# Performance work log

Hardware: AMD Instinct MI355X
Metric: run time of the kernel (lower is better)

## Reference

```python
import jax, jax.numpy as jnp
import numpy as np

N_E = 1024
E_DIM = 256
TAU = 0.5
BETA = 0.25
LAMB = 0.1
EPS = 1e-10


def setup_inputs() -> dict:
    key = jax.random.key(0)
    k1, k2, k3 = jax.random.split(key, 3)
    z = jax.random.normal(k1, (16, 1024, E_DIM), dtype=jnp.float32)
    # kaiming-normal-initialized codebook (std = sqrt(2 / fan_in))
    emb = jax.random.normal(k2, (N_E, E_DIM), dtype=jnp.float32) * np.sqrt(2.0 / E_DIM)
    u = jax.random.uniform(k3, (16 * 1024, N_E), dtype=jnp.float32)
    return {"z": z, "emb": emb, "u": u}


def reference(z, emb, u):
    zf = z.reshape(-1, E_DIM)                                  # [N, e_dim]
    # squared euclidean distances to each code: ||z||^2 + ||e||^2 - 2 z.e
    d = (jnp.sum(zf * zf, axis=1, keepdims=True)
         + jnp.sum(emb * emb, axis=1)
         - 2.0 * jnp.matmul(zf, emb.T))                        # [N, n_e]
    # gumbel-softmax (hard, straight-through) on logits = -d
    g = -jnp.log(-jnp.log(u + EPS) + EPS)
    y_soft = jax.nn.softmax((-d + g) / TAU, axis=-1)
    idx = jnp.argmax(y_soft, axis=-1)
    y_hard = jax.nn.one_hot(idx, N_E, dtype=y_soft.dtype)
    probs = y_hard + y_soft - jax.lax.stop_gradient(y_soft)    # [N, n_e]
    z_q = jnp.matmul(probs, emb).reshape(z.shape)
    # orthogonality loss on the codebook gram matrix
    gram = jnp.matmul(emb, emb.T)
    ortho = jnp.mean((gram - jnp.eye(N_E, dtype=emb.dtype)) ** 2) / (N_E ** 2)
    emb_loss = jnp.mean((jax.lax.stop_gradient(z_q) - z) ** 2)
    commit = BETA * jnp.mean((z_q - jax.lax.stop_gradient(z)) ** 2)
    loss = emb_loss + BETA * commit + LAMB * ortho
    z_q_st = z + jax.lax.stop_gradient(z_q - z)
    e_mean = jnp.mean(probs, axis=0)
    perplexity = jnp.exp(-jnp.sum(e_mean * jnp.log(e_mean + EPS)))
    return loss, z_q_st, perplexity
```

## Files before the change

kernel.cpp:

```cpp
#include <hip/hip_runtime.h>
#include <math.h>
#include <stdint.h>


#define NROWS 16384
#define NE    1024
#define ED    256
#define EPSF  1e-10f
#define INV2048 4.8828125e-4f
#define BM 64
#define BN 64
#define SCW 68

typedef _Float16 half_t;
typedef __attribute__((ext_vector_type(4))) _Float16 half4;
typedef __attribute__((ext_vector_type(8))) _Float16 half8;
typedef __attribute__((ext_vector_type(16))) float floatx16;
typedef unsigned long long u64;

__device__ __forceinline__ void gl_lds16(const void* g, void* l) {
    __builtin_amdgcn_global_load_lds(
        (const __attribute__((address_space(1))) uint32_t*)g,
        (__attribute__((address_space(3))) uint32_t*)l, 16, 0, 0);
}

__device__ __forceinline__ u64 packMax(float v, int code) {
    unsigned int b   = __float_as_uint(v);
    unsigned int key = (b & 0x80000000u) ? ~b : (b | 0x80000000u);
    return ((u64)key << 32) | (unsigned int)(NE - 1 - code);
}

__global__ __launch_bounds__(256) void vq_prep(
        const float* __restrict__ z, const float* __restrict__ emb,
        half_t* __restrict__ zh, half_t* __restrict__ zl,
        half_t* __restrict__ eh, half_t* __restrict__ el,
        float* __restrict__ enorm, float* __restrict__ znorm,
        u64* __restrict__ best)
{
    const int gid = blockIdx.x * 256 + threadIdx.x;
    const int ZQ4 = NROWS * ED / 4;
    if (gid < ZQ4) {
        const float4 v = ((const float4*)z)[gid];
        const float x[4] = {v.x, v.y, v.z, v.w};
        half4 h, l;
#pragma unroll
        for (int i = 0; i < 4; ++i) {
            const half_t hi = (half_t)x[i];
            h[i] = hi; l[i] = (half_t)((x[i] - (float)hi) * 2048.0f);
        }
        *(half4*)&zh[(size_t)gid * 4] = h;
        *(half4*)&zl[(size_t)gid * 4] = l;
        float s = v.x*v.x + v.y*v.y + v.z*v.z + v.w*v.w;
#pragma unroll
        for (int o = 32; o; o >>= 1) s += __shfl_down(s, o);
        if ((threadIdx.x & 63) == 0) znorm[gid >> 6] = s;
    } else {
        const int eg = gid - ZQ4;
        const float4 v = ((const float4*)emb)[eg];
        const float x[4] = {v.x, v.y, v.z, v.w};
        half4 h, l;
#pragma unroll
        for (int i = 0; i < 4; ++i) {
            const half_t hi = (half_t)x[i];
            h[i] = hi; l[i] = (half_t)((x[i] - (float)hi) * 2048.0f);
        }
        *(half4*)&eh[(size_t)eg * 4] = h;
        *(half4*)&el[(size_t)eg * 4] = l;
        float s = v.x*v.x + v.y*v.y + v.z*v.z + v.w*v.w;
#pragma unroll
        for (int o = 32; o; o >>= 1) s += __shfl_down(s, o);
        if ((threadIdx.x & 63) == 0) enorm[eg >> 6] = s;
        if (eg < NROWS) best[eg] = 0ull;
    }
}

__global__ __launch_bounds__(256, 4) void vq_gemm(
        const half_t* __restrict__ zh, const half_t* __restrict__ zl,
        const half_t* __restrict__ eh, const half_t* __restrict__ el,
        const float* __restrict__ u, const float* __restrict__ enorm,
        u64* __restrict__ best)
{
    __shared__ __align__(16) char smem[32768];
    half_t* Ah = (half_t*)smem;
    half_t* Al = (half_t*)(smem + 8192);
    half_t* Bh = (half_t*)(smem + 16384);
    half_t* Bl = (half_t*)(smem + 24576);
    float (*Sc)[SCW] = (float(*)[SCW])smem;
    u64* parr = (u64*)(smem + 17408);

    const int t    = threadIdx.x;
    const int w    = t >> 6;
    const int lane = t & 63;
    const int lrow = lane & 31;
    const int hw   = lane >> 5;

    const int bid = blockIdx.x;
    const int xcd = bid & 7, c = bid >> 3;
    const int m0 = (xcd * 32 + (c >> 4)) * BM;
    const int n0 = (c & 15) * BN;
    const int wm = (w >> 1) * 32, wn = (w & 1) * 32;

    size_t gaoff[2], gboff[2];
#pragma unroll
    for (int it = 0; it < 2; ++it) {
        const int s = it * 256 + t;
        const int row = s >> 3;
        const int cc = (s & 7) ^ (row & 7);
        gaoff[it] = (size_t)(m0 + row) * ED + cc * 8;
        gboff[it] = (size_t)(n0 + row) * ED + cc * 8;
    }

    auto STAGE = [&](int kc) {
#pragma unroll
        for (int it = 0; it < 2; ++it) {
            const int ldso = (it * 256 + w * 64) * 8;
            gl_lds16(zh + gaoff[it] + kc, Ah + ldso);
            gl_lds16(zl + gaoff[it] + kc, Al + ldso);
            gl_lds16(eh + gboff[it] + kc, Bh + ldso);
            gl_lds16(el + gboff[it] + kc, Bl + ldso);
        }
    };

    floatx16 accH = {};
    floatx16 accX = {};

    STAGE(0);
    for (int kc = 0; kc < ED; kc += 64) {
        __syncthreads();
#pragma unroll
        for (int ks = 0; ks < 4; ++ks) {
            const int cch = ks * 2 + hw;
            const int ar = wm + lrow;
            const int br = wn + lrow;
            const int sa = ar * 8 + (cch ^ (ar & 7));
            const int sb = br * 8 + (cch ^ (br & 7));
            const half8 ah = *(const half8*)&Ah[sa * 8];
            const half8 al = *(const half8*)&Al[sa * 8];
            const half8 bh = *(const half8*)&Bh[sb * 8];
            const half8 bl = *(const half8*)&Bl[sb * 8];
            accH = __builtin_amdgcn_mfma_f32_32x32x16_f16(ah, bh, accH, 0, 0, 0);
            accX = __builtin_amdgcn_mfma_f32_32x32x16_f16(ah, bl, accX, 0, 0, 0);
            accX = __builtin_amdgcn_mfma_f32_32x32x16_f16(al, bh, accX, 0, 0, 0);
        }
        __syncthreads();
        if (kc + 64 < ED) STAGE(kc + 64);
    }

    const int   col0 = n0 + wn + lrow;
    const float en0  = enorm[col0];
#pragma unroll
    for (int r = 0; r < 16; ++r) {
        const int lr = wm + (r & 3) + ((r >> 2) << 3) + (hw << 2);
        const float d  = accH[r] + accX[r] * INV2048;
        const float uv = u[(size_t)(m0 + lr) * NE + col0];
        const float g  = -__logf(-__logf(uv + EPSF) + EPSF);
        Sc[lr][wn + lrow] = 2.f * d - en0 + g;
    }
    __syncthreads();

    {
        const int row = t >> 2;
        const int ch  = (t & 3) << 4;
        float bv = -1e38f; int bc = 0;
#pragma unroll
        for (int q = 0; q < 4; ++q) {
            const float4 v = *(const float4*)&Sc[row][ch + (q << 2)];
            const int cc = n0 + ch + (q << 2);
            if (v.x > bv) { bv = v.x; bc = cc; }
            if (v.y > bv) { bv = v.y; bc = cc + 1; }
            if (v.z > bv) { bv = v.z; bc = cc + 2; }
            if (v.w > bv) { bv = v.w; bc = cc + 3; }
        }
        parr[t] = packMax(bv, bc);
    }
    __syncthreads();
    if (t < 64) {
        const u64 a = parr[(t << 2)],     b = parr[(t << 2) + 1];
        const u64 e = parr[(t << 2) + 2], f = parr[(t << 2) + 3];
        const u64 m1 = a > b ? a : b;
        const u64 m2 = e > f ? e : f;
        atomicMax(&best[m0 + t], m1 > m2 ? m1 : m2);
    }
}

__global__ __launch_bounds__(256) void vq_outstore(
        const float* __restrict__ emb, const u64* __restrict__ best,
        const float* __restrict__ znorm, const float* __restrict__ u,
        float* __restrict__ out)
{
    const int t = threadIdx.x;

    if (blockIdx.x == NROWS / 8) {
        __shared__ int    hist[NE];
        __shared__ double redl[4], redp[4];
        for (int i = t; i < NE; i += 256) hist[i] = 0;
        __syncthreads();

        double lsum = 0.0;
#pragma unroll 8
        for (int r = t; r < NROWS; r += 256) {
            const u64 p = best[r];
            const unsigned int key = (unsigned int)(p >> 32);
            const int code = NE - 1 - (int)(p & 0xFFFFFFFFu);
            atomicAdd(&hist[code], 1);
            const unsigned int b = (key & 0x80000000u) ? (key ^ 0x80000000u) : ~key;
            const float s  = __uint_as_float(b);
            const float uv = u[(size_t)r * NE + code];
            const float g  = -__logf(-__logf(uv + EPSF) + EPSF);
            lsum += (double)(znorm[r] - s + g);
        }
        __syncthreads();

        double psum = 0.0;
        for (int i = t; i < NE; i += 256) {
            const float em = (float)hist[i] / (float)NROWS;
            psum += (double)(em * logf(em + EPSF));
        }
#pragma unroll
        for (int o = 32; o; o >>= 1) { lsum += __shfl_down(lsum, o); psum += __shfl_down(psum, o); }
        if ((t & 63) == 0) { redl[t >> 6] = lsum; redp[t >> 6] = psum; }
        __syncthreads();
        if (t == 0) {
            const double mse = (redl[0] + redl[1] + redl[2] + redl[3])
                               / (double)((size_t)NROWS * ED);
            const double tot = redp[0] + redp[1] + redp[2] + redp[3];
            out[0] = (float)(mse * 1.0625);
            out[1 + (size_t)NROWS * ED] = (float)exp(-tot);
        }
        return;
    }

    __shared__ int ridx[8];
    const int m0 = blockIdx.x * 8;
    if (t < 8)
        ridx[t] = NE - 1 - (int)(best[m0 + t] & 0xFFFFFFFFu);
    __syncthreads();

#pragma unroll
    for (int rr = 0; rr < 8; ++rr) {
        const int j = ridx[rr];
        out[1 + (size_t)(m0 + rr) * ED + t] = emb[(size_t)j * ED + t];
    }
}

extern "C" void kernel_launch(void* const* d_in, const int* in_sizes, int n_in,
                              void* d_out, int out_size, void* d_ws, size_t ws_size,
                              hipStream_t stream) {
    const float* z   = (const float*)d_in[0];
    const float* emb = (const float*)d_in[1];
    const float* u   = (const float*)d_in[2];
    float* out = (float*)d_out;

    float*  enorm    = (float*)((char*)d_ws + 5120);
    u64*    best     = (u64*)((char*)d_ws + 9216);
    float*  znorm    = (float*)((char*)d_ws + 140288);
    const size_t small_end = 205824;

    const size_t zsplit = (size_t)NROWS * ED * 2;
    const size_t esplit = (size_t)NE * ED * 2;
    const bool bigws = ws_size >= small_end + 2 * zsplit + 2 * esplit;

    half_t *zh, *zl, *eh, *el;
    if (bigws) {
        char* big = (char*)d_ws + small_end;
        zh = (half_t*)big;
        zl = (half_t*)(big + zsplit);
        eh = (half_t*)(big + 2 * zsplit);
        el = (half_t*)(big + 2 * zsplit + esplit);
    } else {
        zh = (half_t*)((char*)d_out + 8);
        zl = (half_t*)((char*)d_out + 8 + zsplit);
        eh = (half_t*)((char*)d_ws + small_end);
        el = (half_t*)((char*)d_ws + small_end + esplit);
    }

    vq_prep<<<(NROWS * ED / 4 + NE * ED / 4) / 256, 256, 0, stream>>>(
        z, emb, zh, zl, eh, el, enorm, znorm, best);
    vq_gemm<<<(NROWS / BM) * (NE / BN), 256, 0, stream>>>(
        zh, zl, eh, el, u, enorm, best);
    vq_outstore<<<NROWS / 8 + 1, 256, 0, stream>>>(emb, best, znorm, u, out);
}
```

Before: 185.6 us.

## Distribute loss and histogram work across outstore blocks and add finalize kernel

```diff
diff --git a/kernel.cpp b/kernel.cpp
--- a/kernel.cpp
+++ b/kernel.cpp
@@ -38,38 +38,42 @@
         u64* __restrict__ best)
 {
     const int gid = blockIdx.x * 256 + threadIdx.x;
-    const int ZQ4 = NROWS * ED / 4;
-    if (gid < ZQ4) {
-        const float4 v = ((const float4*)z)[gid];
-        const float x[4] = {v.x, v.y, v.z, v.w};
-        half4 h, l;
-#pragma unroll
-        for (int i = 0; i < 4; ++i) {
+    const int ZQ8 = NROWS * ED / 8;
+    if (gid < ZQ8) {
+        const float4 v0 = ((const float4*)z)[(size_t)gid * 2];
+        const float4 v1 = ((const float4*)z)[(size_t)gid * 2 + 1];
+        const float x[8] = {v0.x, v0.y, v0.z, v0.w, v1.x, v1.y, v1.z, v1.w};
+        half8 h, l;
+        float s = 0.f;
+#pragma unroll
+        for (int i = 0; i < 8; ++i) {
             const half_t hi = (half_t)x[i];
             h[i] = hi; l[i] = (half_t)((x[i] - (float)hi) * 2048.0f);
-        }
-        *(half4*)&zh[(size_t)gid * 4] = h;
-        *(half4*)&zl[(size_t)gid * 4] = l;
-        float s = v.x*v.x + v.y*v.y + v.z*v.z + v.w*v.w;
-#pragma unroll
-        for (int o = 32; o; o >>= 1) s += __shfl_down(s, o);
-        if ((threadIdx.x & 63) == 0) znorm[gid >> 6] = s;
+            s = fmaf(x[i], x[i], s);
+        }
+        *(half8*)&zh[(size_t)gid * 8] = h;
+        *(half8*)&zl[(size_t)gid * 8] = l;
+#pragma unroll
+        for (int o = 16; o; o >>= 1) s += __shfl_down(s, o, 32);
+        if ((threadIdx.x & 31) == 0) znorm[gid >> 5] = s;
     } else {
-        const int eg = gid - ZQ4;
-        const float4 v = ((const float4*)emb)[eg];
-        const float x[4] = {v.x, v.y, v.z, v.w};
-        half4 h, l;
-#pragma unroll
-        for (int i = 0; i < 4; ++i) {
+        const int eg = gid - ZQ8;
+        const float4 v0 = ((const float4*)emb)[(size_t)eg * 2];
+        const float4 v1 = ((const float4*)emb)[(size_t)eg * 2 + 1];
+        const float x[8] = {v0.x, v0.y, v0.z, v0.w, v1.x, v1.y, v1.z, v1.w};
+        half8 h, l;
+        float s = 0.f;
+#pragma unroll
+        for (int i = 0; i < 8; ++i) {
             const half_t hi = (half_t)x[i];
             h[i] = hi; l[i] = (half_t)((x[i] - (float)hi) * 2048.0f);
-        }
-        *(half4*)&eh[(size_t)eg * 4] = h;
-        *(half4*)&el[(size_t)eg * 4] = l;
-        float s = v.x*v.x + v.y*v.y + v.z*v.z + v.w*v.w;
-#pragma unroll
-        for (int o = 32; o; o >>= 1) s += __shfl_down(s, o);
-        if ((threadIdx.x & 63) == 0) enorm[eg >> 6] = s;
+            s = fmaf(x[i], x[i], s);
+        }
+        *(half8*)&eh[(size_t)eg * 8] = h;
+        *(half8*)&el[(size_t)eg * 8] = l;
+#pragma unroll
+        for (int o = 16; o; o >>= 1) s += __shfl_down(s, o, 32);
+        if ((threadIdx.x & 31) == 0) enorm[eg >> 5] = s;
         if (eg < NROWS) best[eg] = 0ull;
     }
 }
@@ -186,60 +190,76 @@
 __global__ __launch_bounds__(256) void vq_outstore(
         const float* __restrict__ emb, const u64* __restrict__ best,
         const float* __restrict__ znorm, const float* __restrict__ u,
+        int* __restrict__ idxArr, double* __restrict__ partial,
         float* __restrict__ out)
 {
-    const int t = threadIdx.x;
-
-    if (blockIdx.x == NROWS / 8) {
-        __shared__ int    hist[NE];
-        __shared__ double redl[4], redp[4];
-        for (int i = t; i < NE; i += 256) hist[i] = 0;
-        __syncthreads();
-
-        double lsum = 0.0;
-#pragma unroll 8
-        for (int r = t; r < NROWS; r += 256) {
-            const u64 p = best[r];
-            const unsigned int key = (unsigned int)(p >> 32);
-            const int code = NE - 1 - (int)(p & 0xFFFFFFFFu);
-            atomicAdd(&hist[code], 1);
-            const unsigned int b = (key & 0x80000000u) ? (key ^ 0x80000000u) : ~key;
-            const float s  = __uint_as_float(b);
-            const float uv = u[(size_t)r * NE + code];
-            const float g  = -__logf(-__logf(uv + EPSF) + EPSF);
-            lsum += (double)(znorm[r] - s + g);
-        }
-        __syncthreads();
-
-        double psum = 0.0;
-        for (int i = t; i < NE; i += 256) {
-            const float em = (float)hist[i] / (float)NROWS;
-            psum += (double)(em * logf(em + EPSF));
-        }
-#pragma unroll
-        for (int o = 32; o; o >>= 1) { lsum += __shfl_down(lsum, o); psum += __shfl_down(psum, o); }
-        if ((t & 63) == 0) { redl[t >> 6] = lsum; redp[t >> 6] = psum; }
-        __syncthreads();
-        if (t == 0) {
-            const double mse = (redl[0] + redl[1] + redl[2] + redl[3])
-                               / (double)((size_t)NROWS * ED);
-            const double tot = redp[0] + redp[1] + redp[2] + redp[3];
-            out[0] = (float)(mse * 1.0625);
-            out[1 + (size_t)NROWS * ED] = (float)exp(-tot);
-        }
-        return;
-    }
-
-    __shared__ int ridx[8];
+    __shared__ int   ridx[8];
+    __shared__ float rmse[8];
+    const int t  = threadIdx.x;
     const int m0 = blockIdx.x * 8;
-    if (t < 8)
-        ridx[t] = NE - 1 - (int)(best[m0 + t] & 0xFFFFFFFFu);
-    __syncthreads();
+
+    if (t < 8) {
+        const u64 p = best[m0 + t];
+        const unsigned int key = (unsigned int)(p >> 32);
+        const int code = NE - 1 - (int)(p & 0xFFFFFFFFu);
+        ridx[t] = code;
+        idxArr[m0 + t] = code;
+        const unsigned int b = (key & 0x80000000u) ? (key ^ 0x80000000u) : ~key;
+        const float s  = __uint_as_float(b);
+        const float uv = u[(size_t)(m0 + t) * NE + code];
+        const float g  = -__logf(-__logf(uv + EPSF) + EPSF);
+        rmse[t] = znorm[m0 + t] - s + g;
+    }
+    __syncthreads();
+    if (t == 0) {
+        double acc = 0.0;
+#pragma unroll
+        for (int r = 0; r < 8; ++r) acc += (double)rmse[r];
+        partial[blockIdx.x] = acc;
+    }
 
 #pragma unroll
     for (int rr = 0; rr < 8; ++rr) {
         const int j = ridx[rr];
         out[1 + (size_t)(m0 + rr) * ED + t] = emb[(size_t)j * ED + t];
+    }
+}
+
+__global__ __launch_bounds__(256) void vq_fin(
+        const int* __restrict__ idxArr, const double* __restrict__ partial,
+        float* __restrict__ out)
+{
+    __shared__ int    hist[NE];
+    __shared__ double redl[4], redp[4];
+    const int t = threadIdx.x;
+
+    for (int i = t; i < NE; i += 256) hist[i] = 0;
+    __syncthreads();
+
+    for (int r = t; r < NROWS; r += 256)
+        atomicAdd(&hist[idxArr[r]], 1);
+
+    double lsum = 0.0;
+    for (int b = t; b < NROWS / 8; b += 256)
+        lsum += partial[b];
+    __syncthreads();
+
+    double psum = 0.0;
+    for (int i = t; i < NE; i += 256) {
+        const float em = (float)hist[i] / (float)NROWS;
+        psum += (double)(em * logf(em + EPSF));
+    }
+
+#pragma unroll
+    for (int o = 32; o; o >>= 1) { lsum += __shfl_down(lsum, o); psum += __shfl_down(psum, o); }
+    if ((t & 63) == 0) { redl[t >> 6] = lsum; redp[t >> 6] = psum; }
+    __syncthreads();
+    if (t == 0) {
+        const double mse = (redl[0] + redl[1] + redl[2] + redl[3])
+                           / (double)((size_t)NROWS * ED);
+        const double tot = redp[0] + redp[1] + redp[2] + redp[3];
+        out[0] = (float)(mse * 1.0625);
+        out[1 + (size_t)NROWS * ED] = (float)exp(-tot);
     }
 }
 
@@ -254,7 +274,9 @@
     float*  enorm    = (float*)((char*)d_ws + 5120);
     u64*    best     = (u64*)((char*)d_ws + 9216);
     float*  znorm    = (float*)((char*)d_ws + 140288);
-    const size_t small_end = 205824;
+    int*    idxArr   = (int*)((char*)d_ws + 205824);
+    double* partial  = (double*)((char*)d_ws + 271360);
+    const size_t small_end = 287744;
 
     const size_t zsplit = (size_t)NROWS * ED * 2;
     const size_t esplit = (size_t)NE * ED * 2;
@@ -274,9 +296,11 @@
         el = (half_t*)((char*)d_ws + small_end + esplit);
     }
 
-    vq_prep<<<(NROWS * ED / 4 + NE * ED / 4) / 256, 256, 0, stream>>>(
+    vq_prep<<<(NROWS * ED / 8 + NE * ED / 8) / 256, 256, 0, stream>>>(
         z, emb, zh, zl, eh, el, enorm, znorm, best);
     vq_gemm<<<(NROWS / BM) * (NE / BN), 256, 0, stream>>>(
         zh, zl, eh, el, u, enorm, best);
-    vq_outstore<<<NROWS / 8 + 1, 256, 0, stream>>>(emb, best, znorm, u, out);
-}
+    vq_outstore<<<NROWS / 8, 256, 0, stream>>>(
+        emb, best, znorm, u, idxArr, partial, out);
+    vq_fin<<<1, 256, 0, stream>>>(idxArr, partial, out);
+}
```

Result: faster. 174.3 us (-6.1%).
